# Optimization experiments

Measured on AMD Instinct MI355X. Metric: run time of the kernel, lower is better.

Reference implementation:

```python
import jax, jax.numpy as jnp
import numpy as np

N = 100000
E = 1600000
IN_DIM = 128
OUT_DIM = 128
H = 4
HD = OUT_DIM // H  # 32
NEG_SLOPE = 0.2
EPS_SOFTMAX = 1e-8
EPS_LN = 1e-5


def setup_inputs() -> dict:
    key = jax.random.key(0)
    ks = jax.random.split(key, 6)
    h = jax.random.normal(ks[0], (N, IN_DIM), dtype=jnp.float32)
    edge_index = jax.random.randint(ks[1], (2, E), 0, N, dtype=jnp.int32)
    W = jax.random.normal(ks[2], (IN_DIM, OUT_DIM), dtype=jnp.float32) / np.sqrt(IN_DIM)
    W_self = jax.random.normal(ks[3], (IN_DIM, OUT_DIM), dtype=jnp.float32) / np.sqrt(IN_DIM)
    a_in = jax.random.normal(ks[4], (H, 2 * HD), dtype=jnp.float32) * 0.01
    a_out = jax.random.normal(ks[5], (H, 2 * HD), dtype=jnp.float32) * 0.01
    bias = jnp.zeros((OUT_DIM,), dtype=jnp.float32)
    ln_gamma = jnp.ones((OUT_DIM,), dtype=jnp.float32)
    ln_beta = jnp.zeros((OUT_DIM,), dtype=jnp.float32)
    return {"h": h, "edge_index": edge_index, "W": W, "W_self": W_self,
            "a_in": a_in, "a_out": a_out, "bias": bias,
            "ln_gamma": ln_gamma, "ln_beta": ln_beta}


def _attention_aggregate(h_proj, sender, receiver, attn_vec, num_nodes):
    # h_proj: (N, H, HD); sender/receiver: (E,); attn_vec: (H, 2*HD)
    h_sender = h_proj[sender]      # (E, H, HD)
    h_receiver = h_proj[receiver]  # (E, H, HD)
    # e = sum over concat([h_sender, h_receiver]) * attn_vec, split halves
    e = (jnp.einsum('ehd,hd->eh', h_sender, attn_vec[:, :HD])
         + jnp.einsum('ehd,hd->eh', h_receiver, attn_vec[:, HD:]))
    e = jax.nn.leaky_relu(e, NEG_SLOPE)
    e_max = jax.ops.segment_max(e, receiver, num_segments=num_nodes)  # (N, H)
    alpha = jnp.exp(e - e_max[receiver])
    alpha_sum = jax.ops.segment_sum(alpha, receiver, num_segments=num_nodes)
    alpha = alpha / (alpha_sum[receiver] + EPS_SOFTMAX)
    msg = h_sender * alpha[..., None]  # (E, H, HD)
    return jax.ops.segment_sum(msg, receiver, num_segments=num_nodes)  # (N, H, HD)


def reference(h, edge_index, W, W_self, a_in, a_out, bias, ln_gamma, ln_beta):
    n = h.shape[0]
    h_proj = (h @ W).reshape(n, H, HD)
    h_self = h @ W_self
    src, dst = edge_index[0], edge_index[1]
    h_in = _attention_aggregate(h_proj, src, dst, a_in, n)   # 'in' direction
    h_out = _attention_aggregate(h_proj, dst, src, a_out, n)  # 'out' direction
    combined = h_self + h_in.reshape(n, -1) + h_out.reshape(n, -1) + bias
    mean = combined.mean(axis=-1, keepdims=True)
    var = combined.var(axis=-1, keepdims=True)
    normed = (combined - mean) * jax.lax.rsqrt(var + EPS_LN)
    return normed * ln_gamma + ln_beta
```

## Files before the change

### kernel.cpp

```cpp
#include <hip/hip_runtime.h>
#include <math.h>

#define HEADS 4
#define HD 32
#define DIM 128
#define NEG_SLOPE 0.2f
#define EPS_SM 1e-8f
#define EPS_LN 1e-5f
#define SH1 9
#define PB 256
#define BCOLS 272

typedef _Float16 h2_t __attribute__((ext_vector_type(2)));
typedef _Float16 f16x8 __attribute__((ext_vector_type(8)));
typedef float f32x4 __attribute__((ext_vector_type(4)));

__device__ __forceinline__ float lrelu(float x) { return x > 0.f ? x : NEG_SLOPE * x; }
__device__ __forceinline__ unsigned pkh(float a, float b) {
    return __builtin_bit_cast(unsigned, __builtin_amdgcn_cvt_pkrtz(a, b));
}
__device__ __forceinline__ float dot2(unsigned a, unsigned b, float c) {
    return __builtin_amdgcn_fdot2(__builtin_bit_cast(h2_t, a), __builtin_bit_cast(h2_t, b), c, false);
}
__device__ __forceinline__ float lo16(unsigned u) { return (float)__builtin_bit_cast(h2_t, u)[0]; }
__device__ __forceinline__ float hi16(unsigned u) { return (float)__builtin_bit_cast(h2_t, u)[1]; }

template<int LIM> __device__ __forceinline__ void rsum4(float& a, float& b, float& c, float& d) {
#pragma unroll
    for (int s = 1; s < LIM; s <<= 1) {
        a += __shfl_xor(a, s, 64);
        b += __shfl_xor(b, s, 64);
        c += __shfl_xor(c, s, 64);
        d += __shfl_xor(d, s, 64);
    }
}

__device__ __forceinline__ void dot8(uint4 u, uint4 v, unsigned wpk, float (&acc)[8]) {
    acc[0] = dot2(__builtin_amdgcn_perm(v.x, u.x, 0x05040100u), wpk, acc[0]);
    acc[1] = dot2(__builtin_amdgcn_perm(v.x, u.x, 0x07060302u), wpk, acc[1]);
    acc[2] = dot2(__builtin_amdgcn_perm(v.y, u.y, 0x05040100u), wpk, acc[2]);
    acc[3] = dot2(__builtin_amdgcn_perm(v.y, u.y, 0x07060302u), wpk, acc[3]);
    acc[4] = dot2(__builtin_amdgcn_perm(v.z, u.z, 0x05040100u), wpk, acc[4]);
    acc[5] = dot2(__builtin_amdgcn_perm(v.z, u.z, 0x07060302u), wpk, acc[5]);
    acc[6] = dot2(__builtin_amdgcn_perm(v.w, u.w, 0x05040100u), wpk, acc[6]);
    acc[7] = dot2(__builtin_amdgcn_perm(v.w, u.w, 0x07060302u), wpk, acc[7]);
}

__device__ __forceinline__ void aggr_pairs(int cnt, const int* __restrict__ sdw,
                                           const uint2* __restrict__ wtw,
                                           const char* __restrict__ hpb,
                                           unsigned rowoff, int q, bool hlo, unsigned wsel,
                                           float (&acc)[8]) {
    const int npair = (cnt + 7) >> 3;
#pragma unroll 2
    for (int t = 0; t < npair; ++t) {
        int pi = 4 * t + q;
        uint2 sp = *(const uint2*)&sdw[2 * pi];
        uint4 wp = *(const uint4*)&wtw[2 * pi];
        uint4 u = *(const uint4*)(hpb + (((unsigned)sp.x << 8) + rowoff));
        uint4 v = *(const uint4*)(hpb + (((unsigned)sp.y << 8) + rowoff));
        unsigned wA = hlo ? wp.x : wp.y;
        unsigned wB = hlo ? wp.z : wp.w;
        unsigned wpk = __builtin_amdgcn_perm(wB, wA, wsel);
        dot8(u, v, wpk, acc);
    }
}

__global__ __launch_bounds__(256) void part1a_k(const int* __restrict__ ei, int* __restrict__ cntmat,
                                                int E, int N, int NBIN,
                                                const float* __restrict__ W,
                                                const float* __restrict__ V,
                                                const float* __restrict__ a_in,
                                                const float* __restrict__ a_out,
                                                _Float16* __restrict__ Bt) {
    __shared__ int lcnt[512];
    const int t = threadIdx.x;
    if (blockIdx.x >= PB) {
        int c = (blockIdx.x - PB) * 2 + (t >> 7);
        int k = t & 127;
        float v;
        if (c < 128) {
            v = W[k * 128 + c];
        } else if (c < 256) {
            v = V[k * 128 + (c - 128)];
        } else {
            int d = (c - 256) >> 2, hh = (c - 256) & 3;
            const float* a = (d < 2) ? a_in : a_out;
            int base = hh * 64 + (d & 1) * 32;
            float s = 0.f;
#pragma unroll
            for (int tt = 0; tt < 32; ++tt) s += W[k * 128 + 32 * hh + tt] * a[base + tt];
            v = s;
        }
        Bt[c * 128 + k] = (_Float16)v;
        return;
    }
    const int CH = (E + PB - 1) / PB;
    const int e0 = blockIdx.x * CH;
    const int e1 = min(e0 + CH, E);
    for (int i = t; i < 512; i += 256) lcnt[i] = 0;
    __syncthreads();
    for (int e = e0 + t; e < e1; e += 256) {
        int s = ei[e], d = ei[E + e];
        atomicAdd(&lcnt[d >> SH1], 1);
        atomicAdd(&lcnt[(N + s) >> SH1], 1);
    }
    __syncthreads();
    for (int i = t; i < NBIN; i += 256) cntmat[i * PB + blockIdx.x] = lcnt[i];
}

__global__ __launch_bounds__(256) void scanB_k(const int* __restrict__ cntmat,
                                               int* __restrict__ blkoff, int* __restrict__ btot) {
    __shared__ int ls[PB];
    const int bin = blockIdx.x;
    const int t = threadIdx.x;
    int v = cntmat[bin * PB + t];
    ls[t] = v;
    __syncthreads();
#pragma unroll
    for (int d = 1; d < PB; d <<= 1) {
        int u = (t >= d) ? ls[t - d] : 0;
        __syncthreads();
        ls[t] += u;
        __syncthreads();
    }
    blkoff[bin * PB + t] = ls[t] - v;
    if (t == PB - 1) btot[bin] = ls[t];
}

__global__ __launch_bounds__(256) void scanC_k(const int* __restrict__ btot,
                                               int* __restrict__ bbase, int NBIN, int twoE) {
    __shared__ int ls[256];
    int t = threadIdx.x;
    int i0 = 2 * t, i1 = 2 * t + 1;
    int v0 = (i0 < NBIN) ? btot[i0] : 0;
    int v1 = (i1 < NBIN) ? btot[i1] : 0;
    int pair = v0 + v1;
    ls[t] = pair;
    __syncthreads();
#pragma unroll
    for (int d = 1; d < 256; d <<= 1) {
        int u = (t >= d) ? ls[t - d] : 0;
        __syncthreads();
        ls[t] += u;
        __syncthreads();
    }
    int excl = ls[t] - pair;
    if (i0 < NBIN) bbase[i0] = excl;
    if (i1 < NBIN) bbase[i1] = excl + v0;
    if (t == 0) bbase[NBIN] = twoE;
}

__global__ __launch_bounds__(256) void p1b_gemm_k(const int* __restrict__ ei,
                                                  const int* __restrict__ bbase,
                                                  const int* __restrict__ blkoff,
                                                  unsigned* __restrict__ rec, int E, int N, int NBIN,
                                                  const float* __restrict__ h,
                                                  const _Float16* __restrict__ Bt,
                                                  unsigned* __restrict__ hs_pk,
                                                  unsigned* __restrict__ hp_pk,
                                                  float* __restrict__ pA0, float* __restrict__ pA1,
                                                  float* __restrict__ pB0, float* __restrict__ pB1) {
    __shared__ int gb[512];
    __shared__ int lcur[512];
    __shared__ _Float16 hs[64][128];
    __shared__ _Float16 hss[64][128];

    if (blockIdx.x < PB) {
        const int t = threadIdx.x;
        const int CH = (E + PB - 1) / PB;
        const int e0 = blockIdx.x * CH;
        const int e1 = min(e0 + CH, E);
        for (int i = t; i < 512; i += 256) lcur[i] = 0;
        for (int i = t; i < NBIN; i += 256) gb[i] = bbase[i] + blkoff[i * PB + blockIdx.x];
        __syncthreads();
        for (int e = e0 + t; e < e1; e += 256) {
            int s = ei[e], d = ei[E + e];
            int b1 = d >> SH1;
            int r1 = atomicAdd(&lcur[b1], 1);
            rec[gb[b1] + r1] = (unsigned)s | ((unsigned)(d & 511) << 20);
            int so = N + s;
            int b2 = so >> SH1;
            int r2 = atomicAdd(&lcur[b2], 1);
            rec[gb[b2] + r2] = (unsigned)d | ((unsigned)(so & 511) << 20);
        }
        return;
    }

    const int tid = threadIdx.x;
    const int w = tid >> 6, l = tid & 63;
    const int l15 = l & 15;
    const int kg = l >> 4;
    const int row0 = (blockIdx.x - PB) * 64;
    const int arow = row0 + 16 * w + l15;

    f32x4 acc[17];
#pragma unroll
    for (int j = 0; j < 17; ++j) {
        acc[j][0] = 0.f; acc[j][1] = 0.f; acc[j][2] = 0.f; acc[j][3] = 0.f;
    }

    const uint4* __restrict__ bt4 = (const uint4*)Bt;

#pragma unroll
    for (int kc = 0; kc < 4; ++kc) {
        union { unsigned u[4]; f16x8 v; } cv;
        if (arow < N) {
            float4 x0 = ((const float4*)h)[(size_t)arow * 32 + kc * 8 + kg * 2];
            float4 x1 = ((const float4*)h)[(size_t)arow * 32 + kc * 8 + kg * 2 + 1];
            cv.u[0] = pkh(x0.x, x0.y); cv.u[1] = pkh(x0.z, x0.w);
            cv.u[2] = pkh(x1.x, x1.y); cv.u[3] = pkh(x1.z, x1.w);
        } else {
            cv.u[0] = 0u; cv.u[1] = 0u; cv.u[2] = 0u; cv.u[3] = 0u;
        }
        f16x8 af = cv.v;
#pragma unroll
        for (int j = 0; j < 17; ++j) {
            int col = 16 * j + l15;
            union { uint4 q; f16x8 v; } bc;
            bc.q = bt4[col * 16 + kc * 4 + kg];
            acc[j] = __builtin_amdgcn_mfma_f32_16x16x32_f16(af, bc.v, acc[j], 0, 0, 0);
        }
    }

    const int r4 = kg * 4;
    const int dsel = l15 >> 2, hh = l15 & 3;
    float* __restrict__ pd = (dsel == 0) ? pA0 : (dsel == 1) ? pA1 : (dsel == 2) ? pB0 : pB1;
#pragma unroll
    for (int r = 0; r < 4; ++r) {
        int lr = 16 * w + r4 + r;
        int grow = row0 + lr;
#pragma unroll
        for (int j = 0; j < 8; ++j)
            hs[lr][16 * j + l15] = (_Float16)acc[j][r];
#pragma unroll
        for (int j = 8; j < 16; ++j)
            hss[lr][16 * (j - 8) + l15] = (_Float16)acc[j][r];
        if (grow < N) pd[grow * 4 + hh] = acc[16][r];
    }
    __syncthreads();
    const uint4* hsv = (const uint4*)&hs[0][0];
    const uint4* hssv = (const uint4*)&hss[0][0];
#pragma unroll
    for (int p = 0; p < 4; ++p) {
        int chunk = tid + p * 256;
        int rrow = chunk >> 4, cg = chunk & 15;
        int grow = row0 + rrow;
        if (grow < N) {
            ((uint4*)hp_pk)[(size_t)grow * 16 + cg] = hsv[rrow * 16 + cg];
            ((uint4*)hs_pk)[(size_t)grow * 16 + cg] = hssv[rrow * 16 + cg];
        }
    }
}

__global__ __launch_bounds__(256) void build2_k(const unsigned* __restrict__ rec,
                                                const int* __restrict__ bbase,
                                                int* __restrict__ off, int* __restrict__ csr,
                                                int M, int twoE, int NBIN) {
    __shared__ int lcnt[512];
    __shared__ int lcur[512];
    __shared__ int ls[256];
    const int b = blockIdx.x;
    const int t = threadIdx.x;
    const int base = bbase[b];
    const int cnt = bbase[b + 1] - base;
    const int seg0 = b << SH1;
    for (int i = t; i < 512; i += 256) lcnt[i] = 0;
    __syncthreads();
    for (int k = t; k < cnt; k += 256) atomicAdd(&lcnt[rec[base + k] >> 20], 1);
    __syncthreads();
    int v0 = lcnt[2 * t], v1 = lcnt[2 * t + 1];
    int pair = v0 + v1;
    ls[t] = pair;
    __syncthreads();
#pragma unroll
    for (int d = 1; d < 256; d <<= 1) {
        int u = (t >= d) ? ls[t - d] : 0;
        __syncthreads();
        ls[t] += u;
        __syncthreads();
    }
    int excl = ls[t] - pair;
    lcur[2 * t] = excl;
    lcur[2 * t + 1] = excl + v0;
    int sg = seg0 + 2 * t;
    if (sg < M) off[sg] = base + excl;
    if (sg + 1 < M) off[sg + 1] = base + excl + v0;
    if (b == NBIN - 1 && t == 0) off[M] = twoE;
    __syncthreads();
    for (int k = t; k < cnt; k += 256) {
        unsigned r = rec[base + k];
        int pos = atomicAdd(&lcur[r >> 20], 1);
        csr[base + pos] = (int)(r & 0xFFFFFu);
    }
}

#define ROWLD(x) (*(const uint4*)(hpb + (((unsigned)(x) << 8) + rowoff)))
__global__ __launch_bounds__(256) void node_aggr_ln_k(const unsigned* __restrict__ hp_pk,
                                                      const unsigned* __restrict__ hs_pk,
                                                      const float* __restrict__ pA0, const float* __restrict__ pA1,
                                                      const float* __restrict__ pB0, const float* __restrict__ pB1,
                                                      const int* __restrict__ off, const int* __restrict__ csr,
                                                      const float* __restrict__ bias,
                                                      const float* __restrict__ gamma,
                                                      const float* __restrict__ beta,
                                                      float* __restrict__ out, int N) {
    __shared__ int sds[4][64];
    __shared__ uint2 wts[4][64];
    const int wave = threadIdx.x >> 6;
    const int lane = threadIdx.x & 63;
    const int n = blockIdx.x * 4 + wave;
    if (n >= N) return;
    const int l15 = lane & 15;
    const int q = lane >> 4;
    const unsigned wsel = (l15 & 4) ? 0x07060302u : 0x05040100u;
    const bool hlo = (l15 < 8);
    int* sdw = sds[wave];
    uint2* wtw = wts[wave];
    const char* hpb = (const char*)hp_pk;
    const unsigned rowoff = (unsigned)l15 << 4;

    float acc[8];
#pragma unroll
    for (int k = 0; k < 8; ++k) acc[k] = 0.f;

    const int beg0 = off[n], end0 = off[n + 1];
    const int beg1 = off[N + n], end1 = off[N + n + 1];
    const int len0 = end0 - beg0, len1 = end1 - beg1;

    if (len0 <= 32 && len1 <= 32) {
        const int half = lane >> 5;
        const int hl = lane & 31;
        const int beg = half ? beg1 : beg0;
        const int len = half ? len1 : len0;
        const float* __restrict__ pp0 = half ? pB0 : pA0;
        const float* __restrict__ pp1 = half ? pB1 : pA1;
        float4 r1 = ((const float4*)pp1)[n];
        int sid = 0;
        float e0 = -INFINITY, e1 = -INFINITY, e2 = -INFINITY, e3 = -INFINITY;
        float4 r0 = make_float4(0.f, 0.f, 0.f, 0.f);
        if (hl < len) {
            sid = csr[beg + hl];
            r0 = ((const float4*)pp0)[sid];
        }
        sdw[lane] = 0;
        wtw[lane] = make_uint2(0u, 0u);
        if (hl < len) sdw[half ? len0 + hl : hl] = sid;

        const int cnt = len0 + len1;
        const int npair = (cnt + 7) >> 3;
        uint4 u0 = make_uint4(0u, 0u, 0u, 0u), v0 = u0, u1 = u0, v1 = u0;
        if (npair > 0) {
            uint2 s = *(const uint2*)&sdw[2 * q];
            u0 = ROWLD(s.x); v0 = ROWLD(s.y);
        }
        if (npair > 1) {
            uint2 s = *(const uint2*)&sdw[2 * (4 + q)];
            u1 = ROWLD(s.x); v1 = ROWLD(s.y);
        }

        if (hl < len) {
            e0 = lrelu(r0.x + r1.x);
            e1 = lrelu(r0.y + r1.y);
            e2 = lrelu(r0.z + r1.z);
            e3 = lrelu(r0.w + r1.w);
        }
        float w0 = __expf(e0), w1 = __expf(e1), w2 = __expf(e2), w3 = __expf(e3);
        float s0 = w0, s1 = w1, s2 = w2, s3 = w3;
        const bool small16 = (len0 <= 16 && len1 <= 16);
        if (small16) rsum4<16>(s0, s1, s2, s3);
        else         rsum4<32>(s0, s1, s2, s3);
        w0 *= 1.f / (s0 + EPS_SM);
        w1 *= 1.f / (s1 + EPS_SM);
        w2 *= 1.f / (s2 + EPS_SM);
        w3 *= 1.f / (s3 + EPS_SM);
        if (hl < len)
            wtw[half ? len0 + hl : hl] = make_uint2(pkh(w0, w1), pkh(w2, w3));

        for (int t = 0; t < npair; t += 2) {
            {
                uint4 wp = *(const uint4*)&wtw[2 * (4 * t + q)];
                unsigned wA = hlo ? wp.x : wp.y;
                unsigned wB = hlo ? wp.z : wp.w;
                unsigned wpk = __builtin_amdgcn_perm(wB, wA, wsel);
                dot8(u0, v0, wpk, acc);
            }
            if (t + 2 < npair) {
                uint2 s = *(const uint2*)&sdw[2 * (4 * (t + 2) + q)];
                u0 = ROWLD(s.x); v0 = ROWLD(s.y);
            }
            if (t + 1 < npair) {
                uint4 wp = *(const uint4*)&wtw[2 * (4 * (t + 1) + q)];
                unsigned wA = hlo ? wp.x : wp.y;
                unsigned wB = hlo ? wp.z : wp.w;
                unsigned wpk = __builtin_amdgcn_perm(wB, wA, wsel);
                dot8(u1, v1, wpk, acc);
                if (t + 3 < npair) {
                    uint2 s = *(const uint2*)&sdw[2 * (4 * (t + 3) + q)];
                    u1 = ROWLD(s.x); v1 = ROWLD(s.y);
                }
            }
        }
    } else {
#pragma unroll
        for (int dir = 0; dir < 2; ++dir) {
            const int beg = (dir == 0) ? beg0 : beg1;
            const int end = (dir == 0) ? end0 : end1;
            const int len = end - beg;
            if (len == 0) continue;
            const float* __restrict__ p0 = (dir == 0) ? pA0 : pB0;
            const float* __restrict__ p1 = (dir == 0) ? pA1 : pB1;
            float4 r1 = ((const float4*)p1)[n];

            if (len <= 64) {
                int sid = 0;
                float e0 = -INFINITY, e1 = -INFINITY, e2 = -INFINITY, e3 = -INFINITY;
                if (lane < len) {
                    sid = csr[beg + lane];
                    float4 r0 = ((const float4*)p0)[sid];
                    e0 = lrelu(r0.x + r1.x);
                    e1 = lrelu(r0.y + r1.y);
                    e2 = lrelu(r0.z + r1.z);
                    e3 = lrelu(r0.w + r1.w);
                }
                float w0 = __expf(e0), w1 = __expf(e1), w2 = __expf(e2), w3 = __expf(e3);
                float s0 = w0, s1 = w1, s2 = w2, s3 = w3;
                rsum4<64>(s0, s1, s2, s3);
                w0 *= 1.f / (s0 + EPS_SM);
                w1 *= 1.f / (s1 + EPS_SM);
                w2 *= 1.f / (s2 + EPS_SM);
                w3 *= 1.f / (s3 + EPS_SM);
                sdw[lane] = sid;
                wtw[lane] = make_uint2(pkh(w0, w1), pkh(w2, w3));
                aggr_pairs(len, sdw, wtw, hpb, rowoff, q, hlo, wsel, acc);
            } else {
                float s0 = 0.f, s1 = 0.f, s2 = 0.f, s3 = 0.f;
                for (int base = beg; base < end; base += 64) {
                    int j = base + lane;
                    float e0 = -INFINITY, e1 = -INFINITY, e2 = -INFINITY, e3 = -INFINITY;
                    if (j < end) {
                        int sid = csr[j];
                        float4 r0 = ((const float4*)p0)[sid];
                        e0 = lrelu(r0.x + r1.x);
                        e1 = lrelu(r0.y + r1.y);
                        e2 = lrelu(r0.z + r1.z);
                        e3 = lrelu(r0.w + r1.w);
                    }
                    s0 += __expf(e0); s1 += __expf(e1);
                    s2 += __expf(e2); s3 += __expf(e3);
                }
                rsum4<64>(s0, s1, s2, s3);
                const float is0 = 1.f / (s0 + EPS_SM);
                const float is1 = 1.f / (s1 + EPS_SM);
                const float is2 = 1.f / (s2 + EPS_SM);
                const float is3 = 1.f / (s3 + EPS_SM);
                for (int base = beg; base < end; base += 64) {
                    int cnt = min(64, end - base);
                    int sid = 0;
                    float w0 = 0.f, w1 = 0.f, w2 = 0.f, w3 = 0.f;
                    if (lane < cnt) {
                        sid = csr[base + lane];
                        float4 r0 = ((const float4*)p0)[sid];
                        w0 = __expf(lrelu(r0.x + r1.x)) * is0;
                        w1 = __expf(lrelu(r0.y + r1.y)) * is1;
                        w2 = __expf(lrelu(r0.z + r1.z)) * is2;
                        w3 = __expf(lrelu(r0.w + r1.w)) * is3;
                    }
                    sdw[lane] = sid;
                    wtw[lane] = make_uint2(pkh(w0, w1), pkh(w2, w3));
                    aggr_pairs(cnt, sdw, wtw, hpb, rowoff, q, hlo, wsel, acc);
                }
            }
        }
    }

#pragma unroll
    for (int s = 16; s < 64; s <<= 1) {
#pragma unroll
        for (int k = 0; k < 8; ++k) acc[k] += __shfl_xor(acc[k], s, 64);
    }

    size_t bb = (size_t)n * DIM;
    uint4 hv = ((const uint4*)hs_pk)[(size_t)n * 16 + l15];
    float4 b0 = ((const float4*)bias)[2 * l15];
    float4 b1 = ((const float4*)bias)[2 * l15 + 1];
    float x0 = lo16(hv.x) + acc[0] + b0.x;
    float x1 = hi16(hv.x) + acc[1] + b0.y;
    float x2 = lo16(hv.y) + acc[2] + b0.z;
    float x3 = hi16(hv.y) + acc[3] + b0.w;
    float y0 = lo16(hv.z) + acc[4] + b1.x;
    float y1 = hi16(hv.z) + acc[5] + b1.y;
    float y2 = lo16(hv.w) + acc[6] + b1.z;
    float y3 = hi16(hv.w) + acc[7] + b1.w;
    float sum = x0 + x1 + x2 + x3 + y0 + y1 + y2 + y3;
    float sq = x0 * x0 + x1 * x1 + x2 * x2 + x3 * x3
             + y0 * y0 + y1 * y1 + y2 * y2 + y3 * y3;
#pragma unroll
    for (int m = 1; m < 64; m <<= 1) {
        sum += __shfl_xor(sum, m, 64);
        sq += __shfl_xor(sq, m, 64);
    }
    float mean = sum * (1.f / 512.f);
    float var = sq * (1.f / 512.f) - mean * mean;
    float inv = rsqrtf(var + EPS_LN);
    if (lane < 16) {
        float4 g0 = ((const float4*)gamma)[2 * l15];
        float4 g1 = ((const float4*)gamma)[2 * l15 + 1];
        float4 be0 = ((const float4*)beta)[2 * l15];
        float4 be1 = ((const float4*)beta)[2 * l15 + 1];
        float4 o0 = make_float4((x0 - mean) * inv * g0.x + be0.x,
                                (x1 - mean) * inv * g0.y + be0.y,
                                (x2 - mean) * inv * g0.z + be0.z,
                                (x3 - mean) * inv * g0.w + be0.w);
        float4 o1 = make_float4((y0 - mean) * inv * g1.x + be1.x,
                                (y1 - mean) * inv * g1.y + be1.y,
                                (y2 - mean) * inv * g1.z + be1.z,
                                (y3 - mean) * inv * g1.w + be1.w);
        ((float4*)(out + bb))[2 * l15] = o0;
        ((float4*)(out + bb))[2 * l15 + 1] = o1;
    }
}

extern "C" void kernel_launch(void* const* d_in, const int* in_sizes, int n_in,
                              void* d_out, int out_size, void* d_ws, size_t ws_size,
                              hipStream_t stream) {
    const float* h      = (const float*)d_in[0];
    const int*   ei     = (const int*)d_in[1];
    const float* W      = (const float*)d_in[2];
    const float* W_self = (const float*)d_in[3];
    const float* a_in   = (const float*)d_in[4];
    const float* a_out  = (const float*)d_in[5];
    const float* bias   = (const float*)d_in[6];
    const float* gamma  = (const float*)d_in[7];
    const float* beta   = (const float*)d_in[8];
    float* out = (float*)d_out;

    const int N = in_sizes[0] / DIM;
    const int E = in_sizes[1] / 2;
    const int M = 2 * N;
    const int NBIN = (M + (1 << SH1) - 1) >> SH1;
    const int twoE = 2 * E;

    float* ws = (float*)d_ws;
    size_t off_f = 0;
    unsigned* hs_pk = (unsigned*)(ws + off_f); off_f += (size_t)N * 64;
    unsigned* hp_pk = (unsigned*)(ws + off_f); off_f += (size_t)N * 64;
    float* pA0 = ws + off_f; off_f += (size_t)N * 4;
    float* pA1 = ws + off_f; off_f += (size_t)N * 4;
    float* pB0 = ws + off_f; off_f += (size_t)N * 4;
    float* pB1 = ws + off_f; off_f += (size_t)N * 4;
    int* ip = (int*)(ws + off_f);
    size_t off_i = 0;
    int* cntmat = ip + off_i; off_i += (size_t)NBIN * PB;
    int* blkoff = ip + off_i; off_i += (size_t)NBIN * PB;
    int* btot   = ip + off_i; off_i += NBIN;
    int* bbase  = ip + off_i; off_i += (size_t)NBIN + 1;
    int* off    = ip + off_i; off_i += (size_t)M + 1;
    unsigned* rec = (unsigned*)(ip + off_i); off_i += (size_t)twoE;
    int* csr    = ip + off_i; off_i += (size_t)twoE;
    _Float16* Bt = (_Float16*)(ip + off_i); off_i += (size_t)(BCOLS * 128) / 2;

    const int GB = (N + 63) / 64;

    part1a_k<<<PB + BCOLS / 2, 256, 0, stream>>>(ei, cntmat, E, N, NBIN,
                                                 W, W_self, a_in, a_out, Bt);
    scanB_k<<<NBIN, PB, 0, stream>>>(cntmat, blkoff, btot);
    scanC_k<<<1, 256, 0, stream>>>(btot, bbase, NBIN, twoE);

    p1b_gemm_k<<<PB + GB, 256, 0, stream>>>(ei, bbase, blkoff, rec, E, N, NBIN,
                                            h, Bt, hs_pk, hp_pk, pA0, pA1, pB0, pB1);

    build2_k<<<NBIN, 256, 0, stream>>>(rec, bbase, off, csr, M, twoE, NBIN);

    node_aggr_ln_k<<<(N + 3) / 4, 256, 0, stream>>>(hp_pk, hs_pk, pA0, pA1, pB0, pB1,
                                                    off, csr, bias, gamma, beta, out, N);
}
```

Baseline: 376.2 us.

## Halve CSR bucket size and deepen row-gather prefetch to four pairs

Bucket width for the two-level counting sort drops from 512 to 256 nodes per bin. The bin count doubles, so the shared histograms and the scanC kernel now cover up to 1024 bins, and each bucket-local scan handles one segment per thread. The small-degree aggregation path also issues up to four pairs of neighbour-row gathers before computing softmax weights, instead of two, and unrolls consumption explicitly with prefetch of the next four. This is meant to expose more memory-level parallelism in the gather and shorten per-bucket sort work, at the cost of more registers and larger shared arrays.

```diff
diff --git a/kernel.cpp b/kernel.cpp
--- a/kernel.cpp
+++ b/kernel.cpp
@@ -7,7 +7,7 @@
 #define NEG_SLOPE 0.2f
 #define EPS_SM 1e-8f
 #define EPS_LN 1e-5f
-#define SH1 9
+#define SH1 8
 #define PB 256
 #define BCOLS 272
 
@@ -44,6 +44,14 @@
     acc[5] = dot2(__builtin_amdgcn_perm(v.z, u.z, 0x07060302u), wpk, acc[5]);
     acc[6] = dot2(__builtin_amdgcn_perm(v.w, u.w, 0x05040100u), wpk, acc[6]);
     acc[7] = dot2(__builtin_amdgcn_perm(v.w, u.w, 0x07060302u), wpk, acc[7]);
+}
+
+__device__ __forceinline__ unsigned wpk_at(const uint2* __restrict__ wtw, int pi,
+                                           bool hlo, unsigned wsel) {
+    uint4 wp = *(const uint4*)&wtw[2 * pi];
+    unsigned wA = hlo ? wp.x : wp.y;
+    unsigned wB = hlo ? wp.z : wp.w;
+    return __builtin_amdgcn_perm(wB, wA, wsel);
 }
 
 __device__ __forceinline__ void aggr_pairs(int cnt, const int* __restrict__ sdw,
@@ -56,13 +64,9 @@
     for (int t = 0; t < npair; ++t) {
         int pi = 4 * t + q;
         uint2 sp = *(const uint2*)&sdw[2 * pi];
-        uint4 wp = *(const uint4*)&wtw[2 * pi];
         uint4 u = *(const uint4*)(hpb + (((unsigned)sp.x << 8) + rowoff));
         uint4 v = *(const uint4*)(hpb + (((unsigned)sp.y << 8) + rowoff));
-        unsigned wA = hlo ? wp.x : wp.y;
-        unsigned wB = hlo ? wp.z : wp.w;
-        unsigned wpk = __builtin_amdgcn_perm(wB, wA, wsel);
-        dot8(u, v, wpk, acc);
+        dot8(u, v, wpk_at(wtw, pi, hlo, wsel), acc);
     }
 }
 
@@ -73,7 +77,7 @@
                                                 const float* __restrict__ a_in,
                                                 const float* __restrict__ a_out,
                                                 _Float16* __restrict__ Bt) {
-    __shared__ int lcnt[512];
+    __shared__ int lcnt[1024];
     const int t = threadIdx.x;
     if (blockIdx.x >= PB) {
         int c = (blockIdx.x - PB) * 2 + (t >> 7);
@@ -98,7 +102,7 @@
     const int CH = (E + PB - 1) / PB;
     const int e0 = blockIdx.x * CH;
     const int e1 = min(e0 + CH, E);
-    for (int i = t; i < 512; i += 256) lcnt[i] = 0;
+    for (int i = t; i < 1024; i += 256) lcnt[i] = 0;
     __syncthreads();
     for (int e = e0 + t; e < e1; e += 256) {
         int s = ei[e], d = ei[E + e];
@@ -132,11 +136,14 @@
                                                int* __restrict__ bbase, int NBIN, int twoE) {
     __shared__ int ls[256];
     int t = threadIdx.x;
-    int i0 = 2 * t, i1 = 2 * t + 1;
-    int v0 = (i0 < NBIN) ? btot[i0] : 0;
-    int v1 = (i1 < NBIN) ? btot[i1] : 0;
-    int pair = v0 + v1;
-    ls[t] = pair;
+    int v[4]; int s = 0;
+#pragma unroll
+    for (int j = 0; j < 4; ++j) {
+        int i = 4 * t + j;
+        v[j] = (i < NBIN) ? btot[i] : 0;
+        s += v[j];
+    }
+    ls[t] = s;
     __syncthreads();
 #pragma unroll
     for (int d = 1; d < 256; d <<= 1) {
@@ -145,9 +152,13 @@
         ls[t] += u;
         __syncthreads();
     }
-    int excl = ls[t] - pair;
-    if (i0 < NBIN) bbase[i0] = excl;
-    if (i1 < NBIN) bbase[i1] = excl + v0;
+    int excl = ls[t] - s;
+#pragma unroll
+    for (int j = 0; j < 4; ++j) {
+        int i = 4 * t + j;
+        if (i < NBIN) bbase[i] = excl;
+        excl += v[j];
+    }
     if (t == 0) bbase[NBIN] = twoE;
 }
 
@@ -161,8 +172,8 @@
                                                   unsigned* __restrict__ hp_pk,
                                                   float* __restrict__ pA0, float* __restrict__ pA1,
                                                   float* __restrict__ pB0, float* __restrict__ pB1) {
-    __shared__ int gb[512];
-    __shared__ int lcur[512];
+    __shared__ int gb[1024];
+    __shared__ int lcur[1024];
     __shared__ _Float16 hs[64][128];
     __shared__ _Float16 hss[64][128];
 
@@ -171,18 +182,18 @@
         const int CH = (E + PB - 1) / PB;
         const int e0 = blockIdx.x * CH;
         const int e1 = min(e0 + CH, E);
-        for (int i = t; i < 512; i += 256) lcur[i] = 0;
+        for (int i = t; i < 1024; i += 256) lcur[i] = 0;
         for (int i = t; i < NBIN; i += 256) gb[i] = bbase[i] + blkoff[i * PB + blockIdx.x];
         __syncthreads();
         for (int e = e0 + t; e < e1; e += 256) {
             int s = ei[e], d = ei[E + e];
             int b1 = d >> SH1;
             int r1 = atomicAdd(&lcur[b1], 1);
-            rec[gb[b1] + r1] = (unsigned)s | ((unsigned)(d & 511) << 20);
+            rec[gb[b1] + r1] = (unsigned)s | ((unsigned)(d & 255) << 20);
             int so = N + s;
             int b2 = so >> SH1;
             int r2 = atomicAdd(&lcur[b2], 1);
-            rec[gb[b2] + r2] = (unsigned)d | ((unsigned)(so & 511) << 20);
+            rec[gb[b2] + r2] = (unsigned)d | ((unsigned)(so & 255) << 20);
         }
         return;
     }
@@ -257,21 +268,20 @@
                                                 const int* __restrict__ bbase,
                                                 int* __restrict__ off, int* __restrict__ csr,
                                                 int M, int twoE, int NBIN) {
-    __shared__ int lcnt[512];
-    __shared__ int lcur[512];
+    __shared__ int lcnt[256];
+    __shared__ int lcur[256];
     __shared__ int ls[256];
     const int b = blockIdx.x;
     const int t = threadIdx.x;
     const int base = bbase[b];
     const int cnt = bbase[b + 1] - base;
     const int seg0 = b << SH1;
-    for (int i = t; i < 512; i += 256) lcnt[i] = 0;
+    lcnt[t] = 0;
     __syncthreads();
     for (int k = t; k < cnt; k += 256) atomicAdd(&lcnt[rec[base + k] >> 20], 1);
     __syncthreads();
-    int v0 = lcnt[2 * t], v1 = lcnt[2 * t + 1];
-    int pair = v0 + v1;
-    ls[t] = pair;
+    int v = lcnt[t];
+    ls[t] = v;
     __syncthreads();
 #pragma unroll
     for (int d = 1; d < 256; d <<= 1) {
@@ -280,12 +290,10 @@
         ls[t] += u;
         __syncthreads();
     }
-    int excl = ls[t] - pair;
-    lcur[2 * t] = excl;
-    lcur[2 * t + 1] = excl + v0;
-    int sg = seg0 + 2 * t;
+    int excl = ls[t] - v;
+    lcur[t] = excl;
+    int sg = seg0 + t;
     if (sg < M) off[sg] = base + excl;
-    if (sg + 1 < M) off[sg + 1] = base + excl + v0;
     if (b == NBIN - 1 && t == 0) off[M] = twoE;
     __syncthreads();
     for (int k = t; k < cnt; k += 256) {
@@ -349,15 +357,13 @@
 
         const int cnt = len0 + len1;
         const int npair = (cnt + 7) >> 3;
-        uint4 u0 = make_uint4(0u, 0u, 0u, 0u), v0 = u0, u1 = u0, v1 = u0;
-        if (npair > 0) {
-            uint2 s = *(const uint2*)&sdw[2 * q];
-            u0 = ROWLD(s.x); v0 = ROWLD(s.y);
-        }
-        if (npair > 1) {
-            uint2 s = *(const uint2*)&sdw[2 * (4 + q)];
-            u1 = ROWLD(s.x); v1 = ROWLD(s.y);
-        }
+        uint4 z = make_uint4(0u, 0u, 0u, 0u);
+        uint4 u0 = z, v0 = z, u1 = z, v1 = z, u2 = z, v2 = z, u3 = z, v3 = z;
+        uint2 sp;
+        if (npair > 0) { sp = *(const uint2*)&sdw[2 * q];        u0 = ROWLD(sp.x); v0 = ROWLD(sp.y); }
+        if (npair > 1) { sp = *(const uint2*)&sdw[2 * (4 + q)];  u1 = ROWLD(sp.x); v1 = ROWLD(sp.y); }
+        if (npair > 2) { sp = *(const uint2*)&sdw[2 * (8 + q)];  u2 = ROWLD(sp.x); v2 = ROWLD(sp.y); }
+        if (npair > 3) { sp = *(const uint2*)&sdw[2 * (12 + q)]; u3 = ROWLD(sp.x); v3 = ROWLD(sp.y); }
 
         if (hl < len) {
             e0 = lrelu(r0.x + r1.x);
@@ -377,27 +383,30 @@
         if (hl < len)
             wtw[half ? len0 + hl : hl] = make_uint2(pkh(w0, w1), pkh(w2, w3));
 
-        for (int t = 0; t < npair; t += 2) {
-            {
-                uint4 wp = *(const uint4*)&wtw[2 * (4 * t + q)];
-                unsigned wA = hlo ? wp.x : wp.y;
-                unsigned wB = hlo ? wp.z : wp.w;
-                unsigned wpk = __builtin_amdgcn_perm(wB, wA, wsel);
-                dot8(u0, v0, wpk, acc);
-            }
-            if (t + 2 < npair) {
-                uint2 s = *(const uint2*)&sdw[2 * (4 * (t + 2) + q)];
-                u0 = ROWLD(s.x); v0 = ROWLD(s.y);
-            }
-            if (t + 1 < npair) {
-                uint4 wp = *(const uint4*)&wtw[2 * (4 * (t + 1) + q)];
-                unsigned wA = hlo ? wp.x : wp.y;
-                unsigned wB = hlo ? wp.z : wp.w;
-                unsigned wpk = __builtin_amdgcn_perm(wB, wA, wsel);
-                dot8(u1, v1, wpk, acc);
-                if (t + 3 < npair) {
-                    uint2 s = *(const uint2*)&sdw[2 * (4 * (t + 3) + q)];
-                    u1 = ROWLD(s.x); v1 = ROWLD(s.y);
+        if (npair > 0) {
+            dot8(u0, v0, wpk_at(wtw, q, hlo, wsel), acc);
+            if (npair > 4) { sp = *(const uint2*)&sdw[2 * (16 + q)]; u0 = ROWLD(sp.x); v0 = ROWLD(sp.y); }
+            if (npair > 1) {
+                dot8(u1, v1, wpk_at(wtw, 4 + q, hlo, wsel), acc);
+                if (npair > 5) { sp = *(const uint2*)&sdw[2 * (20 + q)]; u1 = ROWLD(sp.x); v1 = ROWLD(sp.y); }
+                if (npair > 2) {
+                    dot8(u2, v2, wpk_at(wtw, 8 + q, hlo, wsel), acc);
+                    if (npair > 6) { sp = *(const uint2*)&sdw[2 * (24 + q)]; u2 = ROWLD(sp.x); v2 = ROWLD(sp.y); }
+                    if (npair > 3) {
+                        dot8(u3, v3, wpk_at(wtw, 12 + q, hlo, wsel), acc);
+                        if (npair > 7) { sp = *(const uint2*)&sdw[2 * (28 + q)]; u3 = ROWLD(sp.x); v3 = ROWLD(sp.y); }
+                        if (npair > 4) {
+                            dot8(u0, v0, wpk_at(wtw, 16 + q, hlo, wsel), acc);
+                            if (npair > 5) {
+                                dot8(u1, v1, wpk_at(wtw, 20 + q, hlo, wsel), acc);
+                                if (npair > 6) {
+                                    dot8(u2, v2, wpk_at(wtw, 24 + q, hlo, wsel), acc);
+                                    if (npair > 7)
+                                        dot8(u3, v3, wpk_at(wtw, 28 + q, hlo, wsel), acc);
+                                }
+                            }
+                        }
+                    }
                 }
             }
         }
```

Result: no change. 382.5 us (+1.7%).
